# Kernel tuning notes

Measured on AMD Instinct MI355X. Metric: run time of the kernel, lower is better.

The kernel has to match this reference:

```python
import jax, jax.numpy as jnp
import numpy as np

N_NODES = 50000
N_EDGES = 800000
IN_DIM = 8
EDGE_DIM = 4
HIDDEN = 16
OUT_DIM = 1


def _lin_init(key, fan_in, fan_out):
    kw, kb = jax.random.split(key)
    bound = 1.0 / np.sqrt(fan_in)
    W = jax.random.uniform(kw, (fan_in, fan_out), minval=-bound, maxval=bound, dtype=jnp.float32)
    b = jax.random.uniform(kb, (fan_out,), minval=-bound, maxval=bound, dtype=jnp.float32)
    return W, b


def setup_inputs() -> dict:
    key = jax.random.key(0)
    ks = jax.random.split(key, 16)
    x = jax.random.normal(ks[0], (N_NODES, IN_DIM), dtype=jnp.float32)
    edge_index = jax.random.randint(ks[1], (2, N_EDGES), 0, N_NODES, dtype=jnp.int32)
    edge_attr = jax.random.normal(ks[2], (N_EDGES, EDGE_DIM), dtype=jnp.float32)

    inp = {"x": x, "edge_index": edge_index, "edge_attr": edge_attr}
    in_dims = [IN_DIM, HIDDEN]
    for i in range(2):
        d_in = in_dims[i]
        W1, b1 = _lin_init(ks[3 + 4 * i], EDGE_DIM, HIDDEN)
        W2, b2 = _lin_init(ks[4 + 4 * i], HIDDEN, d_in * HIDDEN)
        root = jax.random.uniform(ks[5 + 4 * i], (d_in, HIDDEN), minval=-1.0 / np.sqrt(d_in), maxval=1.0 / np.sqrt(d_in), dtype=jnp.float32)
        bias = jnp.zeros((HIDDEN,), dtype=jnp.float32)
        inp[f"eW1_{i}"] = W1; inp[f"eb1_{i}"] = b1
        inp[f"eW2_{i}"] = W2; inp[f"eb2_{i}"] = b2
        inp[f"root_{i}"] = root; inp[f"bias_{i}"] = bias
    mW1, mb1 = _lin_init(ks[11], HIDDEN, HIDDEN)
    mW2, mb2 = _lin_init(ks[12], HIDDEN, OUT_DIM)
    inp["mW1"] = mW1; inp["mb1"] = mb1; inp["mW2"] = mW2; inp["mb2"] = mb2
    return inp


def _nnconv(x, src, dst, edge_attr, eW1, eb1, eW2, eb2, root, bias):
    # edge MLP -> per-edge weight matrix [E, d_in, HIDDEN]
    h = jax.nn.silu(edge_attr @ eW1 + eb1)
    Wedge = (h @ eW2 + eb2).reshape(edge_attr.shape[0], x.shape[1], HIDDEN)
    # gather source features, per-edge matmul, scatter-mean to targets
    msg = jnp.einsum('ei,eio->eo', x[src], Wedge)  # [E, HIDDEN]
    agg = jax.ops.segment_sum(msg, dst, num_segments=N_NODES)
    cnt = jax.ops.segment_sum(jnp.ones((msg.shape[0],), dtype=msg.dtype), dst, num_segments=N_NODES)
    agg = agg / jnp.maximum(cnt, 1.0)[:, None]
    return x @ root + agg + bias


def reference(x, edge_index, edge_attr,
              eW1_0, eb1_0, eW2_0, eb2_0, root_0, bias_0,
              eW1_1, eb1_1, eW2_1, eb2_1, root_1, bias_1,
              mW1, mb1, mW2, mb2):
    src, dst = edge_index[0], edge_index[1]
    x = jax.nn.relu(_nnconv(x, src, dst, edge_attr, eW1_0, eb1_0, eW2_0, eb2_0, root_0, bias_0))
    x = jax.nn.relu(_nnconv(x, src, dst, edge_attr, eW1_1, eb1_1, eW2_1, eb2_1, root_1, bias_1))
    out = jax.nn.sigmoid(jax.nn.silu(x @ mW1 + mb1) @ mW2 + mb2)
    return out
```

## Files before the change

### kernel.cpp

```cpp
#include <hip/hip_runtime.h>
#include <hip/hip_fp16.h>

#define NN 50000
#define NE 800000
#define NBUCK 392

__device__ __forceinline__ float sigm(float v) { return 1.0f / (1.0f + __expf(-v)); }


__global__ void sort_count(const int* __restrict__ ei,
                           int* __restrict__ cntA, int* __restrict__ cntB)
{
    __shared__ int hA[NBUCK], hB[NBUCK];
    int t = threadIdx.x;
    for (int i = t; i < NBUCK; i += 256) { hA[i] = 0; hB[i] = 0; }
    __syncthreads();
    int base = blockIdx.x * 2048;
#pragma unroll
    for (int r = 0; r < 8; ++r) {
        int idx = base + r * 256 + t;
        if (idx < NE) {
            int s = ei[idx], d = ei[NE + idx];
            atomicAdd(&hB[s >> 7], 1);
            atomicAdd(&hA[d >> 7], 1);
        }
    }
    __syncthreads();
    for (int i = t; i < NBUCK; i += 256) {
        if (hA[i]) atomicAdd(&cntA[i], hA[i]);
        if (hB[i]) atomicAdd(&cntB[i], hB[i]);
    }
}

__global__ void sort_scan(const int* __restrict__ cntA, const int* __restrict__ cntB,
                          int* __restrict__ baseA, int* __restrict__ baseB,
                          int* __restrict__ curA,  int* __restrict__ curB)
{
    __shared__ int a[512], b[512];
    int t = threadIdx.x;
    a[t] = (t < NBUCK) ? cntA[t] : 0;
    b[t] = (t < NBUCK) ? cntB[t] : 0;
    __syncthreads();
#pragma unroll
    for (int dd = 1; dd < 512; dd <<= 1) {
        int av = (t >= dd) ? a[t - dd] : 0;
        int bv = (t >= dd) ? b[t - dd] : 0;
        __syncthreads();
        a[t] += av; b[t] += bv;
        __syncthreads();
    }
    int exA = (t > 0) ? a[t - 1] : 0;
    int exB = (t > 0) ? b[t - 1] : 0;
    if (t < NBUCK) { baseA[t] = exA; curA[t] = exA; baseB[t] = exB; curB[t] = exB; }
    if (t == 511)  { baseA[NBUCK] = a[511]; baseB[NBUCK] = b[511]; }
}

__global__ __launch_bounds__(256) void sort_scatterA(const int* __restrict__ ei,
                                                     int* __restrict__ curA,
                                                     unsigned long long* __restrict__ recA)
{
    __shared__ int lcnt[NBUCK];
    __shared__ int lofs[NBUCK];
    int t = threadIdx.x;
    for (int i = t; i < NBUCK; i += 256) lcnt[i] = 0;
    __syncthreads();
    int base = blockIdx.x * 2048;
#pragma unroll
    for (int r = 0; r < 8; ++r) {
        int e = base + r * 256 + t;
        if (e < NE) atomicAdd(&lcnt[ei[NE + e] >> 7], 1);
    }
    __syncthreads();
    for (int i = t; i < NBUCK; i += 256)
        lofs[i] = lcnt[i] ? atomicAdd(&curA[i], lcnt[i]) : 0;
    __syncthreads();
#pragma unroll
    for (int r = 0; r < 8; ++r) {
        int e = base + r * 256 + t;
        if (e < NE) {
            int s = ei[e], d = ei[NE + e];
            int p = atomicAdd(&lofs[d >> 7], 1);
            recA[p] = ((unsigned long long)(unsigned)(d & 127) << 36)
                    | ((unsigned long long)(unsigned)s << 20)
                    | (unsigned long long)(unsigned)e;
        }
    }
}

__global__ __launch_bounds__(256) void sort_localA(const unsigned long long* __restrict__ recA,
                                                   const int* __restrict__ baseA,
                                                   int* __restrict__ off_all,
                                                   unsigned long long* __restrict__ dlist)
{
    __shared__ int c[128];
    __shared__ int live[128];
    int t = threadIdx.x;
    int b = blockIdx.x;
    int lo = baseA[b], hi = baseA[b + 1];
    if (t < 128) c[t] = 0;
    __syncthreads();
    for (int i = lo + t; i < hi; i += 256)
        atomicAdd(&c[(int)(recA[i] >> 36) & 127], 1);
    __syncthreads();
#pragma unroll
    for (int dd = 1; dd < 128; dd <<= 1) {
        int v = (t >= dd && t < 128) ? c[t - dd] : 0;
        __syncthreads();
        if (t < 128) c[t] += v;
        __syncthreads();
    }
    if (t < 128) {
        int ex = (t > 0) ? c[t - 1] : 0;
        int d = (b << 7) + t;
        if (d <= NN) off_all[d] = lo + ex;
        live[t] = lo + ex;
    }
    __syncthreads();
    for (int i = lo + t; i < hi; i += 256) {
        unsigned long long rec = recA[i];
        int pos = atomicAdd(&live[(int)(rec >> 36) & 127], 1);
        dlist[pos] = rec & 0xFFFFFFFFFull;
    }
}

__global__ __launch_bounds__(256) void sort_scatterB(const unsigned long long* __restrict__ dlist,
                                                     int* __restrict__ curB,
                                                     unsigned long long* __restrict__ recB)
{
    __shared__ int lcnt[NBUCK];
    __shared__ int lofs[NBUCK];
    __shared__ unsigned long long vS[2048];
    int t = threadIdx.x;
    for (int i = t; i < NBUCK; i += 256) lcnt[i] = 0;
    __syncthreads();
    int base = blockIdx.x * 2048;
#pragma unroll
    for (int r = 0; r < 8; ++r) {
        int dp = base + r * 256 + t;
        int li = r * 256 + t;
        if (dp < NE) {
            unsigned long long v = dlist[dp];
            vS[li] = v;
            atomicAdd(&lcnt[(int)(v >> 27) & 511], 1);
        }
    }
    __syncthreads();
    for (int i = t; i < NBUCK; i += 256)
        lofs[i] = lcnt[i] ? atomicAdd(&curB[i], lcnt[i]) : 0;
    __syncthreads();
#pragma unroll
    for (int r = 0; r < 8; ++r) {
        int dp = base + r * 256 + t;
        int li = r * 256 + t;
        if (dp < NE) {
            unsigned long long v = vS[li];
            int s = (int)((v >> 20) & 0xFFFFu);
            int p = atomicAdd(&lofs[s >> 7], 1);
            recB[p] = ((unsigned long long)(unsigned)(s & 127) << 40)
                    | ((unsigned long long)(unsigned)dp << 20)
                    | (v & 0xFFFFFull);
        }
    }
}

__global__ __launch_bounds__(256) void sort_localB(const unsigned long long* __restrict__ recB,
                                                   const int* __restrict__ baseB,
                                                   const float4* __restrict__ ea4,
                                                   int* __restrict__ off_all,
                                                   unsigned* __restrict__ sperm32,
                                                   float4* __restrict__ ea_perm)
{
    __shared__ int c[128];
    __shared__ int live[128];
    int t = threadIdx.x;
    int b = blockIdx.x;
    int lo = baseB[b], hi = baseB[b + 1];
    if (t < 128) c[t] = 0;
    __syncthreads();
    for (int i = lo + t; i < hi; i += 256)
        atomicAdd(&c[(int)(recB[i] >> 40) & 127], 1);
    __syncthreads();
#pragma unroll
    for (int dd = 1; dd < 128; dd <<= 1) {
        int v = (t >= dd && t < 128) ? c[t - dd] : 0;
        __syncthreads();
        if (t < 128) c[t] += v;
        __syncthreads();
    }
    if (t < 128) {
        int ex = (t > 0) ? c[t - 1] : 0;
        int s = (b << 7) + t;
        if (s <= NN) off_all[NN + s] = NE + lo + ex;
        live[t] = lo + ex;
    }
    __syncthreads();
    for (int i = lo + t; i < hi; i += 256) {
        unsigned long long rec = recB[i];
        int k = (int)(rec >> 40) & 127;
        int pos = atomicAdd(&live[k], 1);
        unsigned sl = (unsigned)(k & 15);
        unsigned dp = (unsigned)((rec >> 20) & 0xFFFFFu);
        sperm32[pos] = (sl << 20) | dp;
        ea_perm[pos] = ea4[rec & 0xFFFFFull];
    }
}

template<int DIN>
__global__ __launch_bounds__(256) void edge_fusedG(
        const float* __restrict__ xin,
        const unsigned* __restrict__ sperm32,
        const float4* __restrict__ ea_perm,
        const float* __restrict__ eW1,
        const float* __restrict__ eb1,
        const float* __restrict__ eW2,
        const float* __restrict__ eb2,
        const int*   __restrict__ off_all,
        __half* __restrict__ msgbuf)
{
    constexpr int MROW = 260;
    constexpr int W2B  = DIN * 64 * 16;
    constexpr int SMB  = 16 * MROW * 4 + 256 * 4;
    constexpr int UNIB = (W2B > SMB) ? W2B : SMB;
    __shared__ __align__(16) char uni[UNIB];
    float*  w2Lf  = (float*)uni;
    float*  smemM = (float*)uni;
    int*    sdp   = (int*)(uni + 16 * MROW * 4);
    __shared__ __align__(16) float4 G4[16 * 69];
    __shared__ __align__(16) float4 xbL[16 * 5];
    __shared__ __align__(16) float  xL[16 * DIN];
    __shared__ __align__(16) float  b2L[DIN * 16];
    __shared__ __align__(16) float4 w1t[16];
    __shared__ __align__(16) float  b1s[16];

    int tid = threadIdx.x;
    int nb  = blockIdx.x * 16;
    if (tid < 16) {
        w1t[tid] = make_float4(eW1[tid], eW1[16 + tid], eW1[32 + tid], eW1[48 + tid]);
        b1s[tid] = eb1[tid];
    }
    for (int t = tid; t < 16 * DIN * 16; t += 256) {
        int k = t / (DIN * 16);
        int rem = t - k * DIN * 16;
        int i = rem >> 4, o = rem & 15;
        w2Lf[((((o >> 2) * DIN + i) * 16) + k) * 4 + (o & 3)] = eW2[t];
    }
    for (int t = tid; t < DIN * 16; t += 256) b2L[t] = eb2[t];
    for (int t = tid; t < 16 * DIN; t += 256) xL[t] = xin[(size_t)nb * DIN + t];
    __syncthreads();

    {
        int nl = tid >> 4, k = tid & 15;
        const float* xrow = xL + nl * DIN;
        const float4* w2L4 = (const float4*)uni;
#pragma unroll
        for (int ob = 0; ob < 4; ++ob) {
            float4 a4 = make_float4(0.f, 0.f, 0.f, 0.f);
#pragma unroll
            for (int i = 0; i < DIN; ++i) {
                float4 w = w2L4[(ob * DIN + i) * 16 + k];
                a4.x += xrow[i] * w.x; a4.y += xrow[i] * w.y;
                a4.z += xrow[i] * w.z; a4.w += xrow[i] * w.w;
            }
            G4[nl * 69 + ob * 17 + k] = a4;
        }
        if (k < 4) {
            int ob = k;
            const float4* b2v = (const float4*)b2L;
            float4 a4 = make_float4(0.f, 0.f, 0.f, 0.f);
#pragma unroll
            for (int i = 0; i < DIN; ++i) {
                float4 b = b2v[i * 4 + ob];
                a4.x += xrow[i] * b.x; a4.y += xrow[i] * b.y;
                a4.z += xrow[i] * b.z; a4.w += xrow[i] * b.w;
            }
            xbL[nl * 5 + ob] = a4;
        }
    }
    __syncthreads();

    int eBeg = off_all[NN + nb] - NE;
    int eEnd = off_all[NN + nb + 16] - NE;
    for (int cb = eBeg; cb < eEnd; cb += 256) {
        int pos = cb + tid;
        bool valid = pos < eEnd;
        unsigned pk = valid ? sperm32[pos] : 0u;
        int dp = (int)(pk & 0xFFFFFu);
        int sl = (int)(pk >> 20);
        float4 a = valid ? ea_perm[pos] : make_float4(0.f, 0.f, 0.f, 0.f);

        float h[16];
#pragma unroll
        for (int j = 0; j < 16; ++j) {
            float4 w = w1t[j];
            float p = b1s[j] + a.x * w.x + a.y * w.y + a.z * w.z + a.w * w.w;
            h[j] = p * sigm(p);
        }
        float4 acc[4];
#pragma unroll
        for (int ob = 0; ob < 4; ++ob) acc[ob] = xbL[sl * 5 + ob];
#pragma unroll
        for (int k = 0; k < 16; ++k) {
            float hk = h[k];
#pragma unroll
            for (int ob = 0; ob < 4; ++ob) {
                float4 g = G4[sl * 69 + ob * 17 + k];
                acc[ob].x += hk * g.x; acc[ob].y += hk * g.y;
                acc[ob].z += hk * g.z; acc[ob].w += hk * g.w;
            }
        }
        sdp[tid] = valid ? dp : -1;
#pragma unroll
        for (int ob = 0; ob < 4; ++ob) {
            smemM[(ob * 4 + 0) * MROW + tid] = acc[ob].x;
            smemM[(ob * 4 + 1) * MROW + tid] = acc[ob].y;
            smemM[(ob * 4 + 2) * MROW + tid] = acc[ob].z;
            smemM[(ob * 4 + 3) * MROW + tid] = acc[ob].w;
        }
        __syncthreads();
        int nvalid = eEnd - cb; if (nvalid > 256) nvalid = 256;
        int nr = (nvalid + 31) >> 5;
        for (int r = 0; r < nr; ++r) {
            int le = r * 32 + (tid >> 3);
            int p  = tid & 7;
            int d2 = sdp[le];
            float v0 = smemM[(2 * p)     * MROW + le];
            float v1 = smemM[(2 * p + 1) * MROW + le];
            if (d2 >= 0) {
                __half2 hv = __floats2half2_rn(v0, v1);
                *((__half2*)(msgbuf + (size_t)d2 * 16) + p) = hv;
            }
        }
        __syncthreads();
    }
}

__device__ __forceinline__ float gather_msg16(const __half* __restrict__ msgbuf,
                                              int s0, int e0, int tid)
{
    int half = (tid >> 3) & 1;
    int p    = tid & 7;
    float ax = 0.f, ay = 0.f;
    for (int j = s0 + half; j < e0; j += 2) {
        __half2 hv = *((const __half2*)(msgbuf + (size_t)j * 16) + p);
        float2 f = __half22float2(hv);
        ax += f.x; ay += f.y;
    }
    ax += __shfl_xor(ax, 8, 16);
    ay += __shfl_xor(ay, 8, 16);
    int ch = tid & 15;
    float vx = __shfl(ax, ch >> 1, 16);
    float vy = __shfl(ay, ch >> 1, 16);
    return (ch & 1) ? vy : vx;
}

__global__ __launch_bounds__(256) void gather_L0(
        const float* __restrict__ xin,
        const float* __restrict__ root,
        const float* __restrict__ bias,
        const int*   __restrict__ off_all,
        const __half* __restrict__ msgbuf,
        float* __restrict__ x1)
{
    __shared__ __align__(16) float rootL[8 * 16];
    __shared__ __align__(16) float biasL[16];
    int tid = threadIdx.x;
    if (tid < 128) rootL[tid] = root[tid];
    if (tid < 16) biasL[tid] = bias[tid];
    __syncthreads();

    int ch = tid & 15;
    int n  = blockIdx.x * 16 + (tid >> 4);
    int s0 = off_all[n], e0 = off_all[n + 1];

    float acc = gather_msg16(msgbuf, s0, e0, tid);
    float v = acc / fmaxf((float)(e0 - s0), 1.0f) + biasL[ch];
#pragma unroll
    for (int i = 0; i < 8; ++i)
        v += xin[(size_t)n * 8 + i] * rootL[i * 16 + ch];
    x1[(size_t)n * 16 + ch] = fmaxf(v, 0.f);
}

__global__ __launch_bounds__(256) void gather_final(
        const float* __restrict__ x1,
        const float* __restrict__ root,
        const float* __restrict__ bias,
        const int*   __restrict__ off_all,
        const __half* __restrict__ msgbuf,
        const float* __restrict__ mW1,
        const float* __restrict__ mb1,
        const float* __restrict__ mW2,
        const float* __restrict__ mb2,
        float* __restrict__ out)
{
    __shared__ __align__(16) float rootL[256];
    __shared__ __align__(16) float biasL[16];
    __shared__ __align__(16) float w1m[256];
    __shared__ __align__(16) float b1m[16];
    __shared__ __align__(16) float w2m[16];
    __shared__ float b2m;
    int tid = threadIdx.x;
    rootL[tid] = root[tid];
    w1m[tid] = mW1[tid];
    if (tid < 16) { biasL[tid] = bias[tid]; b1m[tid] = mb1[tid]; w2m[tid] = mW2[tid]; }
    if (tid == 0) b2m = mb2[0];
    __syncthreads();

    int ch = tid & 15;
    int n  = blockIdx.x * 16 + (tid >> 4);
    int s0 = off_all[n], e0 = off_all[n + 1];

    float acc = gather_msg16(msgbuf, s0, e0, tid);
    float v = acc / fmaxf((float)(e0 - s0), 1.0f) + biasL[ch];
#pragma unroll
    for (int i = 0; i < 16; ++i)
        v += x1[(size_t)n * 16 + i] * rootL[i * 16 + ch];
    v = fmaxf(v, 0.f);

    float z = b1m[ch];
#pragma unroll
    for (int o = 0; o < 16; ++o) {
        float vo = __shfl(v, o, 16);
        z += vo * w1m[o * 16 + ch];
    }
    float ss = z * sigm(z) * w2m[ch];
#pragma unroll
    for (int off = 8; off; off >>= 1) ss += __shfl_xor(ss, off, 16);
    if (ch == 0) out[n] = sigm(ss + b2m);
}

extern "C" void kernel_launch(void* const* d_in, const int* in_sizes, int n_in,
                              void* d_out, int out_size, void* d_ws, size_t ws_size,
                              hipStream_t stream) {
    const float* x     = (const float*)d_in[0];
    const int*   ei    = (const int*)  d_in[1];
    const float* ea    = (const float*)d_in[2];
    const float* eW1_0 = (const float*)d_in[3];
    const float* eb1_0 = (const float*)d_in[4];
    const float* eW2_0 = (const float*)d_in[5];
    const float* eb2_0 = (const float*)d_in[6];
    const float* root0 = (const float*)d_in[7];
    const float* bias0 = (const float*)d_in[8];
    const float* eW1_1 = (const float*)d_in[9];
    const float* eb1_1 = (const float*)d_in[10];
    const float* eW2_1 = (const float*)d_in[11];
    const float* eb2_1 = (const float*)d_in[12];
    const float* root1 = (const float*)d_in[13];
    const float* bias1 = (const float*)d_in[14];
    const float* mW1   = (const float*)d_in[15];
    const float* mb1   = (const float*)d_in[16];
    const float* mW2   = (const float*)d_in[17];
    const float* mb2   = (const float*)d_in[18];
    float* out = (float*)d_out;

    const int GG  = NN / 16;
    const int SBK = (NE + 2047) / 2048;

    int* W = (int*)d_ws;
    int* off_all = W;
    int* cntA    = W + 100004;
    int* cntB    = W + 100400;
    int* baseA   = W + 100800;
    int* baseB   = W + 101200;
    int* curA    = W + 101600;
    int* curB    = W + 102000;
    unsigned* sperm32 = (unsigned*)(W + 102400);
    float4* ea_perm   = (float4*)(W + 902400);
    float*  x1        = (float*)(W + 4102400);
    __half* msgbuf    = (__half*)(W + 4902400);
    unsigned long long* recA  = (unsigned long long*)(W + 4902400);
    unsigned long long* dlist = (unsigned long long*)(W + 6502400);
    unsigned long long* recB  = (unsigned long long*)(W + 8102400);

    hipMemsetAsync(cntA, 0, 2 * 396 * sizeof(int), stream);
    sort_count   <<<SBK,   256, 0, stream>>>(ei, cntA, cntB);
    sort_scan    <<<1,     512, 0, stream>>>(cntA, cntB, baseA, baseB, curA, curB);
    sort_scatterA<<<SBK,   256, 0, stream>>>(ei, curA, recA);
    sort_localA  <<<NBUCK, 256, 0, stream>>>(recA, baseA, off_all, dlist);
    sort_scatterB<<<SBK,   256, 0, stream>>>(dlist, curB, recB);
    sort_localB  <<<NBUCK, 256, 0, stream>>>(recB, baseB, (const float4*)ea,
                                             off_all, sperm32, ea_perm);

    edge_fusedG<8><<<GG, 256, 0, stream>>>(x, sperm32, ea_perm, eW1_0, eb1_0,
                                           eW2_0, eb2_0, off_all, msgbuf);
    gather_L0<<<GG, 256, 0, stream>>>(x, root0, bias0, off_all, msgbuf, x1);

    edge_fusedG<16><<<GG, 256, 0, stream>>>(x1, sperm32, ea_perm, eW1_1, eb1_1,
                                            eW2_1, eb2_1, off_all, msgbuf);
    gather_final<<<GG, 256, 0, stream>>>(x1, root1, bias1, off_all, msgbuf,
                                         mW1, mb1, mW2, mb2, out);
}
```

Before: 289.4 us.

## Write messages in source-sorted order and gather via dst-to-position index

```diff
diff --git a/kernel.cpp b/kernel.cpp
--- a/kernel.cpp
+++ b/kernel.cpp
@@ -167,7 +167,7 @@
                                                    const int* __restrict__ baseB,
                                                    const float4* __restrict__ ea4,
                                                    int* __restrict__ off_all,
-                                                   unsigned* __restrict__ sperm32,
+                                                   unsigned* __restrict__ spos,
                                                    float4* __restrict__ ea_perm)
 {
     __shared__ int c[128];
@@ -198,9 +198,8 @@
         unsigned long long rec = recB[i];
         int k = (int)(rec >> 40) & 127;
         int pos = atomicAdd(&live[k], 1);
-        unsigned sl = (unsigned)(k & 15);
         unsigned dp = (unsigned)((rec >> 20) & 0xFFFFFu);
-        sperm32[pos] = (sl << 20) | dp;
+        spos[dp] = (unsigned)pos;
         ea_perm[pos] = ea4[rec & 0xFFFFFull];
     }
 }
@@ -208,7 +207,6 @@
 template<int DIN>
 __global__ __launch_bounds__(256) void edge_fusedG(
         const float* __restrict__ xin,
-        const unsigned* __restrict__ sperm32,
         const float4* __restrict__ ea_perm,
         const float* __restrict__ eW1,
         const float* __restrict__ eb1,
@@ -217,20 +215,14 @@
         const int*   __restrict__ off_all,
         __half* __restrict__ msgbuf)
 {
-    constexpr int MROW = 260;
-    constexpr int W2B  = DIN * 64 * 16;
-    constexpr int SMB  = 16 * MROW * 4 + 256 * 4;
-    constexpr int UNIB = (W2B > SMB) ? W2B : SMB;
-    __shared__ __align__(16) char uni[UNIB];
-    float*  w2Lf  = (float*)uni;
-    float*  smemM = (float*)uni;
-    int*    sdp   = (int*)(uni + 16 * MROW * 4);
+    __shared__ __align__(16) float4 w2L4[4 * DIN * 17];
     __shared__ __align__(16) float4 G4[16 * 69];
     __shared__ __align__(16) float4 xbL[16 * 5];
     __shared__ __align__(16) float  xL[16 * DIN];
     __shared__ __align__(16) float  b2L[DIN * 16];
     __shared__ __align__(16) float4 w1t[16];
     __shared__ __align__(16) float  b1s[16];
+    __shared__ int eoffL[17];
 
     int tid = threadIdx.x;
     int nb  = blockIdx.x * 16;
@@ -238,11 +230,15 @@
         w1t[tid] = make_float4(eW1[tid], eW1[16 + tid], eW1[32 + tid], eW1[48 + tid]);
         b1s[tid] = eb1[tid];
     }
-    for (int t = tid; t < 16 * DIN * 16; t += 256) {
-        int k = t / (DIN * 16);
-        int rem = t - k * DIN * 16;
-        int i = rem >> 4, o = rem & 15;
-        w2Lf[((((o >> 2) * DIN + i) * 16) + k) * 4 + (o & 3)] = eW2[t];
+    if (tid < 17) eoffL[tid] = off_all[NN + nb + tid] - NE;
+    {
+        float* w2f = (float*)w2L4;
+        for (int t = tid; t < 16 * DIN * 16; t += 256) {
+            int k = t / (DIN * 16);
+            int rem = t - k * DIN * 16;
+            int i = rem >> 4, o = rem & 15;
+            w2f[((((o >> 2) * DIN + i) * 17) + k) * 4 + (o & 3)] = eW2[t];
+        }
     }
     for (int t = tid; t < DIN * 16; t += 256) b2L[t] = eb2[t];
     for (int t = tid; t < 16 * DIN; t += 256) xL[t] = xin[(size_t)nb * DIN + t];
@@ -251,13 +247,12 @@
     {
         int nl = tid >> 4, k = tid & 15;
         const float* xrow = xL + nl * DIN;
-        const float4* w2L4 = (const float4*)uni;
 #pragma unroll
         for (int ob = 0; ob < 4; ++ob) {
             float4 a4 = make_float4(0.f, 0.f, 0.f, 0.f);
 #pragma unroll
             for (int i = 0; i < DIN; ++i) {
-                float4 w = w2L4[(ob * DIN + i) * 16 + k];
+                float4 w = w2L4[(ob * DIN + i) * 17 + k];
                 a4.x += xrow[i] * w.x; a4.y += xrow[i] * w.y;
                 a4.z += xrow[i] * w.z; a4.w += xrow[i] * w.w;
             }
@@ -278,15 +273,17 @@
     }
     __syncthreads();
 
-    int eBeg = off_all[NN + nb] - NE;
-    int eEnd = off_all[NN + nb + 16] - NE;
-    for (int cb = eBeg; cb < eEnd; cb += 256) {
-        int pos = cb + tid;
-        bool valid = pos < eEnd;
-        unsigned pk = valid ? sperm32[pos] : 0u;
-        int dp = (int)(pk & 0xFFFFFu);
-        int sl = (int)(pk >> 20);
-        float4 a = valid ? ea_perm[pos] : make_float4(0.f, 0.f, 0.f, 0.f);
+    int eBeg = eoffL[0];
+    int eEnd = eoffL[16];
+    for (int pos = eBeg + tid; pos < eEnd; pos += 256) {
+        int loI = 0, hiI = 16;
+#pragma unroll
+        for (int stp = 0; stp < 4; ++stp) {
+            int mid = (loI + hiI) >> 1;
+            if (pos >= eoffL[mid]) loI = mid; else hiI = mid;
+        }
+        int sl = loI;
+        float4 a = ea_perm[pos];
 
         float h[16];
 #pragma unroll
@@ -308,40 +305,34 @@
                 acc[ob].z += hk * g.z; acc[ob].w += hk * g.w;
             }
         }
-        sdp[tid] = valid ? dp : -1;
-#pragma unroll
-        for (int ob = 0; ob < 4; ++ob) {
-            smemM[(ob * 4 + 0) * MROW + tid] = acc[ob].x;
-            smemM[(ob * 4 + 1) * MROW + tid] = acc[ob].y;
-            smemM[(ob * 4 + 2) * MROW + tid] = acc[ob].z;
-            smemM[(ob * 4 + 3) * MROW + tid] = acc[ob].w;
-        }
-        __syncthreads();
-        int nvalid = eEnd - cb; if (nvalid > 256) nvalid = 256;
-        int nr = (nvalid + 31) >> 5;
-        for (int r = 0; r < nr; ++r) {
-            int le = r * 32 + (tid >> 3);
-            int p  = tid & 7;
-            int d2 = sdp[le];
-            float v0 = smemM[(2 * p)     * MROW + le];
-            float v1 = smemM[(2 * p + 1) * MROW + le];
-            if (d2 >= 0) {
-                __half2 hv = __floats2half2_rn(v0, v1);
-                *((__half2*)(msgbuf + (size_t)d2 * 16) + p) = hv;
-            }
-        }
-        __syncthreads();
+        __half2 h01 = __floats2half2_rn(acc[0].x, acc[0].y);
+        __half2 h23 = __floats2half2_rn(acc[0].z, acc[0].w);
+        __half2 h45 = __floats2half2_rn(acc[1].x, acc[1].y);
+        __half2 h67 = __floats2half2_rn(acc[1].z, acc[1].w);
+        __half2 h89 = __floats2half2_rn(acc[2].x, acc[2].y);
+        __half2 hAB = __floats2half2_rn(acc[2].z, acc[2].w);
+        __half2 hCD = __floats2half2_rn(acc[3].x, acc[3].y);
+        __half2 hEF = __floats2half2_rn(acc[3].z, acc[3].w);
+        uint4 w0 = make_uint4(*(unsigned*)&h01, *(unsigned*)&h23,
+                              *(unsigned*)&h45, *(unsigned*)&h67);
+        uint4 w1 = make_uint4(*(unsigned*)&h89, *(unsigned*)&hAB,
+                              *(unsigned*)&hCD, *(unsigned*)&hEF);
+        uint4* dst = (uint4*)(msgbuf + (size_t)pos * 16);
+        dst[0] = w0;
+        dst[1] = w1;
     }
 }
 
 __device__ __forceinline__ float gather_msg16(const __half* __restrict__ msgbuf,
+                                              const unsigned* __restrict__ spos,
                                               int s0, int e0, int tid)
 {
     int half = (tid >> 3) & 1;
     int p    = tid & 7;
     float ax = 0.f, ay = 0.f;
     for (int j = s0 + half; j < e0; j += 2) {
-        __half2 hv = *((const __half2*)(msgbuf + (size_t)j * 16) + p);
+        unsigned sp = spos[j];
+        __half2 hv = *((const __half2*)(msgbuf + (size_t)sp * 16) + p);
         float2 f = __half22float2(hv);
         ax += f.x; ay += f.y;
     }
@@ -358,6 +349,7 @@
         const float* __restrict__ root,
         const float* __restrict__ bias,
         const int*   __restrict__ off_all,
+        const unsigned* __restrict__ spos,
         const __half* __restrict__ msgbuf,
         float* __restrict__ x1)
 {
@@ -372,7 +364,7 @@
     int n  = blockIdx.x * 16 + (tid >> 4);
     int s0 = off_all[n], e0 = off_all[n + 1];
 
-    float acc = gather_msg16(msgbuf, s0, e0, tid);
+    float acc = gather_msg16(msgbuf, spos, s0, e0, tid);
     float v = acc / fmaxf((float)(e0 - s0), 1.0f) + biasL[ch];
 #pragma unroll
     for (int i = 0; i < 8; ++i)
@@ -385,6 +377,7 @@
         const float* __restrict__ root,
         const float* __restrict__ bias,
         const int*   __restrict__ off_all,
+        const unsigned* __restrict__ spos,
         const __half* __restrict__ msgbuf,
         const float* __restrict__ mW1,
         const float* __restrict__ mb1,
@@ -409,7 +402,7 @@
     int n  = blockIdx.x * 16 + (tid >> 4);
     int s0 = off_all[n], e0 = off_all[n + 1];
 
-    float acc = gather_msg16(msgbuf, s0, e0, tid);
+    float acc = gather_msg16(msgbuf, spos, s0, e0, tid);
     float v = acc / fmaxf((float)(e0 - s0), 1.0f) + biasL[ch];
 #pragma unroll
     for (int i = 0; i < 16; ++i)
@@ -463,8 +456,8 @@
     int* baseB   = W + 101200;
     int* curA    = W + 101600;
     int* curB    = W + 102000;
-    unsigned* sperm32 = (unsigned*)(W + 102400);
-    float4* ea_perm   = (float4*)(W + 902400);
+    float4* ea_perm   = (float4*)(W + 102400);
+    unsigned* spos    = (unsigned*)(W + 3302400);
     float*  x1        = (float*)(W + 4102400);
     __half* msgbuf    = (__half*)(W + 4902400);
     unsigned long long* recA  = (unsigned long long*)(W + 4902400);
@@ -472,20 +465,20 @@
     unsigned long long* recB  = (unsigned long long*)(W + 8102400);
 
     hipMemsetAsync(cntA, 0, 2 * 396 * sizeof(int), stream);
-    sort_count   <<<SBK,   256, 0, stream>>>(ei, cntA, cntB);
-    sort_scan    <<<1,     512, 0, stream>>>(cntA, cntB, baseA, baseB, curA, curB);
-    sort_scatterA<<<SBK,   256, 0, stream>>>(ei, curA, recA);
-    sort_localA  <<<NBUCK, 256, 0, stream>>>(recA, baseA, off_all, dlist);
-    sort_scatterB<<<SBK,   256, 0, stream>>>(dlist, curB, recB);
-    sort_localB  <<<NBUCK, 256, 0, stream>>>(recB, baseB, (const float4*)ea,
-                                             off_all, sperm32, ea_perm);
-
-    edge_fusedG<8><<<GG, 256, 0, stream>>>(x, sperm32, ea_perm, eW1_0, eb1_0,
+    sort_count   <<<SBK,  256, 0, stream>>>(ei, cntA, cntB);
+    sort_scan    <<<1,    512, 0, stream>>>(cntA, cntB, baseA, baseB, curA, curB);
+    sort_scatterA<<<SBK,  256, 0, stream>>>(ei, curA, recA);
+    sort_localA  <<<NBUCK,256, 0, stream>>>(recA, baseA, off_all, dlist);
+    sort_scatterB<<<SBK,  256, 0, stream>>>(dlist, curB, recB);
+    sort_localB  <<<NBUCK,256, 0, stream>>>(recB, baseB, (const float4*)ea,
+                                            off_all, spos, ea_perm);
+
+    edge_fusedG<8><<<GG, 256, 0, stream>>>(x, ea_perm, eW1_0, eb1_0,
                                            eW2_0, eb2_0, off_all, msgbuf);
-    gather_L0<<<GG, 256, 0, stream>>>(x, root0, bias0, off_all, msgbuf, x1);
-
-    edge_fusedG<16><<<GG, 256, 0, stream>>>(x1, sperm32, ea_perm, eW1_1, eb1_1,
+    gather_L0<<<GG, 256, 0, stream>>>(x, root0, bias0, off_all, spos, msgbuf, x1);
+
+    edge_fusedG<16><<<GG, 256, 0, stream>>>(x1, ea_perm, eW1_1, eb1_1,
                                             eW2_1, eb2_1, off_all, msgbuf);
-    gather_final<<<GG, 256, 0, stream>>>(x1, root1, bias1, off_all, msgbuf,
+    gather_final<<<GG, 256, 0, stream>>>(x1, root1, bias1, off_all, spos, msgbuf,
                                          mW1, mb1, mW2, mb2, out);
 }
```

Result: slower. 308.5 us (+6.6%).
